# Kernel tuning notes

Hardware: AMD Instinct MI355X
Metric: run time of the kernel (lower is better)

The kernel has to match this reference:

```python
import jax, jax.numpy as jnp
import numpy as np
import math

D_MODEL = 512
NHEAD = 8
D_K = D_MODEL // NHEAD
FACTOR = 5


def setup_inputs() -> dict:
    key = jax.random.key(0)
    ks = jax.random.split(key, 9)
    B, L = 2, 2048
    s = 1.0 / math.sqrt(D_MODEL)
    inp = {
        "x": jax.random.normal(ks[0], (B, L, D_MODEL), dtype=jnp.float32),
        "Wq": jax.random.normal(ks[1], (D_MODEL, D_MODEL), dtype=jnp.float32) * s,
        "bq": jnp.zeros((D_MODEL,), dtype=jnp.float32),
        "Wk": jax.random.normal(ks[2], (D_MODEL, D_MODEL), dtype=jnp.float32) * s,
        "bk": jnp.zeros((D_MODEL,), dtype=jnp.float32),
        "Wv": jax.random.normal(ks[3], (D_MODEL, D_MODEL), dtype=jnp.float32) * s,
        "bv": jnp.zeros((D_MODEL,), dtype=jnp.float32),
        "Wo": jax.random.normal(ks[4], (D_MODEL, D_MODEL), dtype=jnp.float32) * s,
        "bo": jnp.zeros((D_MODEL,), dtype=jnp.float32),
    }
    return inp


def reference(x, Wq, bq, Wk, bk, Wv, bv, Wo, bo):
    B, L, _ = x.shape
    # u keys kept per query (static: depends only on static L)
    u = min(L, int(FACTOR * math.log(L)) if L > 1 else L)

    def proj(W, b):
        # [B,L,D] -> [B,H,L,d_k]
        y = x @ W.T + b
        return y.reshape(B, L, NHEAD, D_K).transpose(0, 2, 1, 3)

    Q = proj(Wq, bq)
    K = proj(Wk, bk)
    V = proj(Wv, bv)

    scores = jnp.einsum("bhqd,bhkd->bhqk", Q, K) / math.sqrt(D_K)  # [B,H,L,L]
    # topk thresholding: keep only scores >= u-th largest per query row
    topk_vals, _ = jax.lax.top_k(scores, u)
    thresh = topk_vals[..., -1:]
    scores = jnp.where(scores < thresh, -10000.0, scores)
    attn = jax.nn.softmax(scores, axis=-1)  # dropout disabled (p=0 / eval)
    out = jnp.einsum("bhqk,bhkd->bhqd", attn, V)  # [B,H,L,d_k]
    out = out.transpose(0, 2, 1, 3).reshape(B, L, D_MODEL)
    return out @ Wo.T + bo
```

## Files before the change

### kernel.cpp

```cpp
#include <hip/hip_runtime.h>
#include <hip/hip_fp16.h>
#include <math.h>

#define LSEQ   2048
#define DMODEL 512
#define NHEAD  8
#define DK     64
#define UK     38

typedef __attribute__((ext_vector_type(8))) _Float16 v8h;
typedef __attribute__((ext_vector_type(4))) _Float16 v4h;
typedef __attribute__((ext_vector_type(4))) float    v4f;

__device__ __forceinline__ unsigned long long mapu64(double x){
    unsigned long long s = (unsigned long long)__double_as_longlong(x);
    return (s & 0x8000000000000000ull) ? ~s : (s | 0x8000000000000000ull);
}
__device__ __forceinline__ unsigned map32(float x){
    unsigned s = __float_as_uint(x);
    return (s & 0x80000000u) ? ~s : (s | 0x80000000u);
}
__device__ __forceinline__ float unmap32(unsigned u){
    unsigned s = (u & 0x80000000u) ? (u & 0x7fffffffu) : ~u;
    return __uint_as_float(s);
}
__device__ __forceinline__ unsigned map16(unsigned h){
    return (h & 0x8000u) ? ((~h) & 0xFFFFu) : (h | 0x8000u);
}

__global__ __launch_bounds__(256) void split_hl(
    const float* __restrict__ X,  const float* __restrict__ Wq,
    const float* __restrict__ Wk, const float* __restrict__ Wv,
    _Float16* __restrict__ Xh, _Float16* __restrict__ Xl,
    _Float16* __restrict__ Whl)
{
    const int idx = blockIdx.x * 256 + threadIdx.x;
    const int NXQ = (4096 * 512) / 4;
    const float* __restrict__ src;
    _Float16* __restrict__ dh;
    _Float16* __restrict__ dl;
    size_t off;
    if (idx < NXQ){
        src = X; dh = Xh; dl = Xl; off = (size_t)idx * 4;
    } else {
        int wi = idx - NXQ;
        int m  = wi >> 16;
        src = (m == 0) ? Wq : (m == 1 ? Wk : Wv);
        dh  = Whl + (size_t)m * 524288;
        dl  = dh + 262144;
        off = (size_t)(wi & 65535) * 4;
    }
    float4 v = *(const float4*)&src[off];
    v4h h, l;
    h[0] = (_Float16)v.x; l[0] = (_Float16)(v.x - (float)h[0]);
    h[1] = (_Float16)v.y; l[1] = (_Float16)(v.y - (float)h[1]);
    h[2] = (_Float16)v.z; l[2] = (_Float16)(v.z - (float)h[2]);
    h[3] = (_Float16)v.w; l[3] = (_Float16)(v.w - (float)h[3]);
    *(v4h*)&dh[off] = h;
    *(v4h*)&dl[off] = l;
}

__global__ __launch_bounds__(256) void qkv_f16(
    const _Float16* __restrict__ Xh, const _Float16* __restrict__ Xl,
    const _Float16* __restrict__ Whl,
    const float* __restrict__ bq, const float* __restrict__ bk,
    const float* __restrict__ bv,
    double* __restrict__ qD, double* __restrict__ kRow,
    __half* __restrict__ qH, __half* __restrict__ kH, float* __restrict__ vB)
{
    const int mode = blockIdx.z;
    const _Float16* __restrict__ Wh = Whl + (size_t)mode * 524288;
    const _Float16* __restrict__ Wl = Wh + 262144;
    const float* __restrict__ bias = (mode == 0) ? bq : (mode == 1 ? bk : bv);
    const int r0 = blockIdx.x * 64, c0 = blockIdx.y * 64;
    __shared__ _Float16 Ah[64][72], Al[64][72];
    __shared__ _Float16 Bh[64][72], Bl[64][72];
    const int tid  = threadIdx.x;
    const int lane = tid & 63, wv = tid >> 6;
    const int m0   = wv << 4;
    const int row  = lane & 15, kq = lane >> 4;

    v4f acc[4] = {};

    for (int kb = 0; kb < DMODEL; kb += 64){
        __syncthreads();
        #pragma unroll
        for (int it = 0; it < 2; ++it){
            int slot = it * 256 + tid;
            int m = slot >> 3, o8 = (slot & 7) << 3;
            size_t ga = (size_t)(r0 + m) * DMODEL + kb + o8;
            size_t gb = (size_t)(c0 + m) * DMODEL + kb + o8;
            *(v8h*)&Ah[m][o8] = *(const v8h*)&Xh[ga];
            *(v8h*)&Al[m][o8] = *(const v8h*)&Xl[ga];
            *(v8h*)&Bh[m][o8] = *(const v8h*)&Wh[gb];
            *(v8h*)&Bl[m][o8] = *(const v8h*)&Wl[gb];
        }
        __syncthreads();
        v8h ah0 = *(const v8h*)&Ah[m0 + row][kq * 8];
        v8h ah1 = *(const v8h*)&Ah[m0 + row][kq * 8 + 32];
        v8h al0 = *(const v8h*)&Al[m0 + row][kq * 8];
        v8h al1 = *(const v8h*)&Al[m0 + row][kq * 8 + 32];
        #pragma unroll
        for (int j = 0; j < 4; ++j){
            const int j0 = j << 4;
            v8h bh0 = *(const v8h*)&Bh[j0 + row][kq * 8];
            v8h bh1 = *(const v8h*)&Bh[j0 + row][kq * 8 + 32];
            v8h bl0 = *(const v8h*)&Bl[j0 + row][kq * 8];
            v8h bl1 = *(const v8h*)&Bl[j0 + row][kq * 8 + 32];
            acc[j] = __builtin_amdgcn_mfma_f32_16x16x32_f16(ah0, bh0, acc[j], 0, 0, 0);
            acc[j] = __builtin_amdgcn_mfma_f32_16x16x32_f16(ah0, bl0, acc[j], 0, 0, 0);
            acc[j] = __builtin_amdgcn_mfma_f32_16x16x32_f16(al0, bh0, acc[j], 0, 0, 0);
            acc[j] = __builtin_amdgcn_mfma_f32_16x16x32_f16(ah1, bh1, acc[j], 0, 0, 0);
            acc[j] = __builtin_amdgcn_mfma_f32_16x16x32_f16(ah1, bl1, acc[j], 0, 0, 0);
            acc[j] = __builtin_amdgcn_mfma_f32_16x16x32_f16(al1, bh1, acc[j], 0, 0, 0);
        }
    }

    const int h = c0 >> 6;
    #pragma unroll
    for (int j = 0; j < 4; ++j){
        const int dk = (j << 4) + row;
        const float bi = bias[c0 + dk];
        #pragma unroll
        for (int rr = 0; rr < 4; ++rr){
            const int r = r0 + m0 + (kq << 2) + rr;
            const int bidx = r >> 11, l = r & 2047;
            const size_t rowb = (size_t)(bidx * NHEAD + h) * LSEQ + l;
            float v = acc[j][rr] + bi;
            if (mode == 0){
                double vd = (double)v * 0.125;
                qD[rowb * DK + dk] = vd;
                ((_Float16*)qH)[rowb * DK + dk] = (_Float16)vd;
            } else if (mode == 1){
                kRow[rowb * DK + dk] = (double)v;
                ((_Float16*)kH)[rowb * DK + dk] = (_Float16)v;
            } else {
                vB[rowb * DK + dk] = v;
            }
        }
    }
}

__global__ __launch_bounds__(256) void gemm_f32(
    const float* __restrict__ X, const float* __restrict__ W,
    const float* __restrict__ bias, float* __restrict__ out)
{
    const int r0 = blockIdx.x * 64, c0 = blockIdx.y * 64;
    __shared__ float Xs[32][68];
    __shared__ float Ws[32][68];
    const int tid = threadIdx.x;
    const int tx = tid & 15, ty = tid >> 4;
    float acc[4][4] = {};
    for (int kb = 0; kb < DMODEL; kb += 32){
        __syncthreads();
        #pragma unroll
        for (int i = 0; i < 2; ++i){
            int f4 = i * 256 + tid;
            int m = f4 >> 3, kg = (f4 & 7) << 2;
            float4 xv = *(const float4*)&X[(r0 + m) * DMODEL + kb + kg];
            Xs[kg+0][m] = xv.x; Xs[kg+1][m] = xv.y; Xs[kg+2][m] = xv.z; Xs[kg+3][m] = xv.w;
            float4 wv = *(const float4*)&W[(c0 + m) * DMODEL + kb + kg];
            Ws[kg+0][m] = wv.x; Ws[kg+1][m] = wv.y; Ws[kg+2][m] = wv.z; Ws[kg+3][m] = wv.w;
        }
        __syncthreads();
        #pragma unroll
        for (int kk = 0; kk < 32; ++kk){
            float4 av = *(const float4*)&Xs[kk][ty << 2];
            float4 bv = *(const float4*)&Ws[kk][tx << 2];
            float a[4] = {av.x, av.y, av.z, av.w};
            float b[4] = {bv.x, bv.y, bv.z, bv.w};
            #pragma unroll
            for (int ii = 0; ii < 4; ++ii)
                #pragma unroll
                for (int jj = 0; jj < 4; ++jj)
                    acc[ii][jj] = fmaf(a[ii], b[jj], acc[ii][jj]);
        }
    }
    #pragma unroll
    for (int ii = 0; ii < 4; ++ii){
        int r = r0 + (ty << 2) + ii;
        float4 o;
        o.x = acc[ii][0] + bias[c0 + (tx << 2) + 0];
        o.y = acc[ii][1] + bias[c0 + (tx << 2) + 1];
        o.z = acc[ii][2] + bias[c0 + (tx << 2) + 2];
        o.w = acc[ii][3] + bias[c0 + (tx << 2) + 3];
        *(float4*)&out[(size_t)r * DMODEL + c0 + (tx << 2)] = o;
    }
}

__global__ __launch_bounds__(256) void score_gemm(
    const __half* __restrict__ qH, const __half* __restrict__ kH,
    __half* __restrict__ Sh, const int bh0)
{
    const int bh = bh0 + blockIdx.z;
    const int r0 = blockIdx.x * 64, c0 = blockIdx.y * 64;
    __shared__ _Float16 Qs[64][72];
    __shared__ _Float16 Ks[64][72];
    const int tid = threadIdx.x;
    const int lane = tid & 63, wv = tid >> 6;
    const size_t qb = ((size_t)bh * LSEQ + r0) * DK;
    const size_t kb = ((size_t)bh * LSEQ + c0) * DK;
    #pragma unroll
    for (int i = 0; i < 2; ++i){
        int c = i * 256 + tid;
        int m = c >> 3, off8 = (c & 7) << 3;
        *(v8h*)&Qs[m][off8] = *(const v8h*)&qH[qb + (size_t)m * DK + off8];
        *(v8h*)&Ks[m][off8] = *(const v8h*)&kH[kb + (size_t)m * DK + off8];
    }
    __syncthreads();
    const int m0 = wv << 4;
    const int row = lane & 15, kq = lane >> 4;
    v8h a0 = *(const v8h*)&Qs[m0 + row][kq * 8];
    v8h a1 = *(const v8h*)&Qs[m0 + row][kq * 8 + 32];
    #pragma unroll
    for (int j0 = 0; j0 < 64; j0 += 16){
        v8h b0 = *(const v8h*)&Ks[j0 + row][kq * 8];
        v8h b1 = *(const v8h*)&Ks[j0 + row][kq * 8 + 32];
        v4f acc = {0.f, 0.f, 0.f, 0.f};
        acc = __builtin_amdgcn_mfma_f32_16x16x32_f16(a0, b0, acc, 0, 0, 0);
        acc = __builtin_amdgcn_mfma_f32_16x16x32_f16(a1, b1, acc, 0, 0, 0);
        #pragma unroll
        for (int r = 0; r < 4; ++r){
            int gr = r0 + m0 + kq * 4 + r;
            int gc = c0 + j0 + row;
            unsigned hbits = (unsigned)__half_as_ushort((__half)acc[r]);
            unsigned short key = (unsigned short)map16(hbits);
            ((unsigned short*)Sh)[((size_t)blockIdx.z * LSEQ + gr) * LSEQ + gc] = key;
        }
    }
}

__device__ __forceinline__ void finish_common(
    const int ncand, const int gl, const int bh, const int lane,
    const double qd, const double* __restrict__ kRow, const float* __restrict__ vB,
    float* __restrict__ ctx, int* __restrict__ jlsR, float* __restrict__ wlsR,
    double* __restrict__ sLds)
{
    const unsigned long long mlt = (1ull << lane) - 1ull;
    if (lane >= ncand) jlsR[lane] = 0;
    if (lane < 4) jlsR[64 + lane] = 0;
    int myJ = jlsR[lane];

    double q8[8];
    #pragma unroll
    for (int k = 0; k < 8; ++k) q8[k] = __shfl(qd, (lane & 7) + (k << 3));
    const int grp = lane >> 3, dl = lane & 7;
    const size_t kb = (size_t)bh * LSEQ;

    double kbf[8];
    {
        int j0 = __shfl(myJ, grp);
        const double* __restrict__ kr = &kRow[(kb + j0) * DK + dl];
        #pragma unroll
        for (int k = 0; k < 8; ++k) kbf[k] = kr[k << 3];
    }
    #pragma unroll
    for (int p = 0; p < 8; ++p){
        double nbf[8];
        if (p < 7){
            int jn = __shfl(myJ, ((p + 1) << 3) + grp);
            const double* __restrict__ krn = &kRow[(kb + jn) * DK + dl];
            #pragma unroll
            for (int k = 0; k < 8; ++k) nbf[k] = krn[k << 3];
        }
        double s = 0.0;
        #pragma unroll
        for (int k = 0; k < 8; ++k) s = fma(q8[k], kbf[k], s);
        s += __shfl_xor(s, 1); s += __shfl_xor(s, 2); s += __shfl_xor(s, 4);
        if (dl == 0) sLds[(p << 3) + grp] = s;
        #pragma unroll
        for (int k = 0; k < 8; ++k) kbf[k] = nbf[k];
    }
    double myS = (lane < ncand) ? sLds[lane] : -1.0e308;

    unsigned long long cu = (lane < ncand) ? mapu64(myS) : 0ull;
    unsigned long long T64 = 0ull;
    for (int bit = 63; bit >= 0; --bit){
        unsigned long long Tp = T64 | (1ull << bit);
        int c = __popcll(__ballot(cu >= Tp));
        if (c >= UK){ T64 = Tp; if (c == UK) break; }
    }
    const bool sel = (cu >= T64);

    double xm = sel ? myS : -1.0e308;
    #pragma unroll
    for (int off = 32; off; off >>= 1) xm = fmax(xm, __shfl_xor(xm, off));
    float w = sel ? expf((float)(myS - xm)) : 0.0f;
    float z = w;
    #pragma unroll
    for (int off = 32; off; off >>= 1) z += __shfl_xor(z, off);
    unsigned long long bm = __ballot(sel);
    int p = __popcll(bm & mlt);
    if (sel){ wlsR[p] = w; jlsR[p] = myJ; }
    const int cnt = __popcll(bm);
    const float invZ = 1.0f / z;

    if (lane >= cnt) wlsR[lane] = 0.0f;
    if (lane < 4){ wlsR[64 + lane] = 0.0f; jlsR[64 + lane] = 0; }

    const float* __restrict__ vsl = vB + (size_t)bh * (LSEQ * DK);
    float o = 0.0f;
    for (int e0 = 0; e0 < cnt; e0 += 16){
        float w16[16]; int j16[16];
        #pragma unroll
        for (int t = 0; t < 16; ++t){ w16[t] = wlsR[e0 + t]; j16[t] = jlsR[e0 + t]; }
        float v16[16];
        #pragma unroll
        for (int t = 0; t < 16; ++t) v16[t] = vsl[(size_t)j16[t] * DK + lane];
        #pragma unroll
        for (int t = 0; t < 16; ++t) o = fmaf(w16[t], v16[t], o);
    }
    ctx[((size_t)(bh >> 3) * LSEQ + gl) * DMODEL + (bh & 7) * DK + lane] = o * invZ;
}

__device__ __forceinline__ void finish_row_f32(
    float (&acc)[32], const int gl, const int bh, const int lane, const float margin,
    const double qd, const double* __restrict__ kRow, const float* __restrict__ vB,
    float* __restrict__ ctx, int* __restrict__ jlsR, float* __restrict__ wlsR,
    double* __restrict__ sLds)
{
    unsigned u[32];
    #pragma unroll
    for (int ch = 0; ch < 32; ++ch) u[ch] = map32(acc[ch]);
    unsigned T = 0u; int curc = 2048;
    for (int bit = 31; bit >= 0; --bit){
        unsigned Tp = T | (1u << bit);
        int c = 0;
        #pragma unroll
        for (int ch = 0; ch < 32; ++ch) c += __popcll(__ballot(u[ch] >= Tp));
        if (c >= UK){ T = Tp; curc = c; }
        if (curc <= 48) break;
    }
    const unsigned Tlo = map32(unmap32(T) - margin);
    const unsigned long long mlt = (1ull << lane) - 1ull;
    int base = 0;
    #pragma unroll
    for (int ch = 0; ch < 32; ++ch){
        bool sel = (u[ch] >= Tlo);
        unsigned long long bm = __ballot(sel);
        int p = base + __popcll(bm & mlt);
        if (sel && p < 64) jlsR[p] = (ch << 6) + lane;
        base += __popcll(bm);
    }
    const int ncand = base > 64 ? 64 : base;
    finish_common(ncand, gl, bh, lane, qd, kRow, vB, ctx, jlsR, wlsR, sLds);
}

__global__ __launch_bounds__(256) void select_kernel(
    const __half* __restrict__ Sh, const double* __restrict__ qD,
    const double* __restrict__ kRow, const float* __restrict__ vB,
    float* __restrict__ ctx, const int bh0)
{
    __shared__ int    jls[4][68];
    __shared__ float  wls[4][68];
    __shared__ double sds[4][64];
    const int tid = threadIdx.x, lane = tid & 63, wv = tid >> 6;
    const int rgS = blockIdx.x * 4 + wv;
    const int bh = bh0 + (rgS >> 11), l = rgS & 2047;
    const double qd = qD[((size_t)bh * LSEQ + l) * DK + lane];
    unsigned u[32];
    const unsigned short* __restrict__ Srow =
        (const unsigned short*)Sh + (size_t)rgS * LSEQ;
    #pragma unroll
    for (int it = 0; it < 4; ++it){
        uint4 v = *(const uint4*)&Srow[it * 512 + (lane << 3)];
        unsigned ws[4] = {v.x, v.y, v.z, v.w};
        #pragma unroll
        for (int q = 0; q < 4; ++q){
            u[it*8 + 2*q]     = ws[q] & 0xFFFFu;
            u[it*8 + 2*q + 1] = ws[q] >> 16;
        }
    }
    unsigned T = 0u; int curc = 2048;
    for (int bit = 15; bit >= 0; --bit){
        unsigned Tp = T | (1u << bit);
        int c = 0;
        #pragma unroll
        for (int ch = 0; ch < 32; ++ch) c += __popcll(__ballot(u[ch] >= Tp));
        if (c >= UK){ T = Tp; curc = c; }
        if (curc <= 48) break;
    }
    unsigned hb = (T & 0x8000u) ? (T & 0x7FFFu) : ((~T) & 0xFFFFu);
    float tf = __half2float(__ushort_as_half((unsigned short)hb)) - 2.2e-2f;
    unsigned short tlb = __half_as_ushort(__float2half_rd(tf));
    const unsigned Tlo = map16(tlb);

    const unsigned long long mlt = (1ull << lane) - 1ull;
    int base = 0;
    #pragma unroll
    for (int ch = 0; ch < 32; ++ch){
        bool sel = (u[ch] >= Tlo);
        unsigned long long bm = __ballot(sel);
        int p = base + __popcll(bm & mlt);
        int j = ((ch >> 3) << 9) + (lane << 3) + (ch & 7);
        if (sel && p < 64) jls[wv][p] = j;
        base += __popcll(bm);
    }
    const int ncand = base > 64 ? 64 : base;
    finish_common(ncand, l, bh, lane, qd, kRow, vB, ctx,
                  &jls[wv][0], &wls[wv][0], &sds[wv][0]);
}

__global__ __launch_bounds__(256) void attn_kernel(
    const double* __restrict__ qD, const double* __restrict__ kRow,
    const float* __restrict__ vB, float* __restrict__ ctx)
{
    __shared__ float2 Kld2[16 * 66];
    __shared__ float  qsf[8][64];
    __shared__ int    jls[8][68];
    __shared__ float  wlsf[8][68];
    __shared__ double sds[8][64];

    const int tid = threadIdx.x, lane = tid & 63, wv = tid >> 6;
    const int bh = blockIdx.x >> 8;
    const int l0 = (blockIdx.x & 255) << 3;
    const int rA = l0 + (wv << 1), rB = rA + 1;

    for (int e = tid; e < 512; e += 256){
        int r = e >> 6, d = e & 63;
        qsf[r][d] = (float)qD[((size_t)bh * LSEQ + l0 + r) * DK + d];
    }
    const double qdA = qD[((size_t)bh * LSEQ + rA) * DK + lane];
    const double qdB = qD[((size_t)bh * LSEQ + rB) * DK + lane];

    float accA[32] = {}, accB[32] = {};
    const size_t kBase = (size_t)bh * (LSEQ * DK);

    for (int dh = 0; dh < 2; ++dh){
        __syncthreads();
        float qa[32], qb[32];
        #pragma unroll
        for (int i = 0; i < 8; ++i){
            float4 va = *(const float4*)&qsf[wv << 1][dh * 32 + i * 4];
            qa[i*4+0]=va.x; qa[i*4+1]=va.y; qa[i*4+2]=va.z; qa[i*4+3]=va.w;
            float4 vb4 = *(const float4*)&qsf[(wv << 1) + 1][dh * 32 + i * 4];
            qb[i*4+0]=vb4.x; qb[i*4+1]=vb4.y; qb[i*4+2]=vb4.z; qb[i*4+3]=vb4.w;
        }
        #pragma unroll
        for (int ch = 0; ch < 32; ++ch){
            const int cb = ch << 6;
            __syncthreads();
            #pragma unroll
            for (int i = 0; i < 4; ++i){
                int j   = i * 16 + (wv << 2) + (lane >> 4);
                int dpl = lane & 15;
                double2 kd = *(const double2*)&kRow[kBase + (size_t)(cb + j) * DK + dh * 32 + dpl * 2];
                Kld2[dpl * 66 + j] = make_float2((float)kd.x, (float)kd.y);
            }
            __syncthreads();
            float a0 = accA[ch], b0 = accB[ch];
            #pragma unroll
            for (int dpl = 0; dpl < 16; ++dpl){
                float2 k = Kld2[dpl * 66 + lane];
                a0 = fmaf(qa[2*dpl],   k.x, a0);
                a0 = fmaf(qa[2*dpl+1], k.y, a0);
                b0 = fmaf(qb[2*dpl],   k.x, b0);
                b0 = fmaf(qb[2*dpl+1], k.y, b0);
            }
            accA[ch] = a0; accB[ch] = b0;
        }
    }

    finish_row_f32(accA, rA, bh, lane, 1e-3f, qdA, kRow, vB, ctx,
                   &jls[wv<<1][0], &wlsf[wv<<1][0], &sds[wv<<1][0]);
    finish_row_f32(accB, rB, bh, lane, 1e-3f, qdB, kRow, vB, ctx,
                   &jls[(wv<<1)+1][0], &wlsf[(wv<<1)+1][0], &sds[(wv<<1)+1][0]);
}

extern "C" void kernel_launch(void* const* d_in, const int* in_sizes, int n_in,
                              void* d_out, int out_size, void* d_ws, size_t ws_size,
                              hipStream_t stream)
{
    const float* x  = (const float*)d_in[0];
    const float* Wq = (const float*)d_in[1];
    const float* bq = (const float*)d_in[2];
    const float* Wk = (const float*)d_in[3];
    const float* bk = (const float*)d_in[4];
    const float* Wv = (const float*)d_in[5];
    const float* bv = (const float*)d_in[6];
    const float* Wo = (const float*)d_in[7];
    const float* bo = (const float*)d_in[8];
    float* out = (float*)d_out;
    char* ws = (char*)d_ws;
    const size_t MiB = 1024 * 1024;
    double* qD   = (double*)(ws);
    double* kRow = (double*)(ws + 16 * MiB);
    float*  vB   = (float*) (ws + 32 * MiB);
    float*  ctx  = (float*) (ws + 40 * MiB);
    __half* qH   = (__half*)(ws + 48 * MiB);
    __half* kH   = (__half*)(ws + 52 * MiB);
    __half* Sh   = (__half*)(ws + 56 * MiB);
    _Float16* Xh  = (_Float16*)(ws + 40 * MiB);
    _Float16* Xl  = (_Float16*)(ws + 44 * MiB);
    _Float16* Whl = (_Float16*)(ws + 56 * MiB);
    size_t avail = (ws_size > 56 * MiB) ? (ws_size - 56 * MiB) : 0;
    int slab = (int)(avail / (8 * MiB)); if (slab > 16) slab = 16;

    dim3 blk(256);
    split_hl<<<dim3(2816), blk, 0, stream>>>(x, Wq, Wk, Wv, Xh, Xl, Whl);
    qkv_f16 <<<dim3(64, 8, 3), blk, 0, stream>>>(Xh, Xl, Whl, bq, bk, bv,
                                                 qD, kRow, qH, kH, vB);
    if (slab >= 1){
        for (int s0 = 0; s0 < NHEAD * 2; s0 += slab){
            int nb = NHEAD * 2 - s0; if (nb > slab) nb = slab;
            score_gemm   <<<dim3(32, 32, nb), blk, 0, stream>>>(qH, kH, Sh, s0);
            select_kernel<<<dim3(nb * 512),   blk, 0, stream>>>(Sh, qD, kRow, vB, ctx, s0);
        }
    } else {
        attn_kernel<<<dim3(4096), blk, 0, stream>>>(qD, kRow, vB, ctx);
    }
    gemm_f32<<<dim3(64, 8), blk, 0, stream>>>(ctx, Wo, bo, out);
}
```

Baseline: 279.1 us.

## Replace bitwise radix threshold search with LDS histogram select in select_kernel

The per-row top-k threshold search used a 16-step bitwise loop, where each step ran 32 ballots over the row's fp16 keys. It is replaced with a 256-bin LDS histogram on the high byte, a wave prefix scan to find the bin holding the k-th largest key, and a bitwise search over only the keys in that bin. The old loop is kept as a fallback when that bin holds more than 64 keys. Separately, finish_common's software-pipelined K gather over a fixed 8 chunks becomes a simple loop over only ncand candidates, giving up prefetch overlap in exchange for skipping unused chunks. The histogram adds LDS atomics whose contention depends on how the keys are distributed, and the finished threshold can differ slightly from the old search's early-exit threshold.

```diff
diff --git a/kernel.cpp b/kernel.cpp
--- a/kernel.cpp
+++ b/kernel.cpp
@@ -246,30 +246,14 @@
     for (int k = 0; k < 8; ++k) q8[k] = __shfl(qd, (lane & 7) + (k << 3));
     const int grp = lane >> 3, dl = lane & 7;
     const size_t kb = (size_t)bh * LSEQ;
-
-    double kbf[8];
-    {
-        int j0 = __shfl(myJ, grp);
-        const double* __restrict__ kr = &kRow[(kb + j0) * DK + dl];
-        #pragma unroll
-        for (int k = 0; k < 8; ++k) kbf[k] = kr[k << 3];
-    }
-    #pragma unroll
-    for (int p = 0; p < 8; ++p){
-        double nbf[8];
-        if (p < 7){
-            int jn = __shfl(myJ, ((p + 1) << 3) + grp);
-            const double* __restrict__ krn = &kRow[(kb + jn) * DK + dl];
-            #pragma unroll
-            for (int k = 0; k < 8; ++k) nbf[k] = krn[k << 3];
-        }
+    for (int e0 = 0; e0 < ncand; e0 += 8){
+        int j = jlsR[e0 + grp];
+        const double* __restrict__ kr = &kRow[(kb + j) * DK + dl];
         double s = 0.0;
         #pragma unroll
-        for (int k = 0; k < 8; ++k) s = fma(q8[k], kbf[k], s);
+        for (int k = 0; k < 8; ++k) s = fma(q8[k], kr[k << 3], s);
         s += __shfl_xor(s, 1); s += __shfl_xor(s, 2); s += __shfl_xor(s, 4);
-        if (dl == 0) sLds[(p << 3) + grp] = s;
-        #pragma unroll
-        for (int k = 0; k < 8; ++k) kbf[k] = nbf[k];
+        if (dl == 0) sLds[e0 + grp] = s;
     }
     double myS = (lane < ncand) ? sLds[lane] : -1.0e308;
 
@@ -351,13 +335,21 @@
     const double* __restrict__ kRow, const float* __restrict__ vB,
     float* __restrict__ ctx, const int bh0)
 {
-    __shared__ int    jls[4][68];
-    __shared__ float  wls[4][68];
-    __shared__ double sds[4][64];
+    __shared__ int      jls[4][68];
+    __shared__ float    wls[4][68];
+    __shared__ double   sds[4][64];
+    __shared__ unsigned hist[4][256];
+    __shared__ unsigned cbuf[4][64];
+    __shared__ unsigned ccnt[4];
     const int tid = threadIdx.x, lane = tid & 63, wv = tid >> 6;
     const int rgS = blockIdx.x * 4 + wv;
     const int bh = bh0 + (rgS >> 11), l = rgS & 2047;
     const double qd = qD[((size_t)bh * LSEQ + l) * DK + lane];
+
+    #pragma unroll
+    for (int k = 0; k < 4; ++k) hist[wv][(lane << 2) + k] = 0u;
+    if (lane == 0) ccnt[wv] = 0u;
+
     unsigned u[32];
     const unsigned short* __restrict__ Srow =
         (const unsigned short*)Sh + (size_t)rgS * LSEQ;
@@ -371,15 +363,66 @@
             u[it*8 + 2*q + 1] = ws[q] >> 16;
         }
     }
-    unsigned T = 0u; int curc = 2048;
-    for (int bit = 15; bit >= 0; --bit){
-        unsigned Tp = T | (1u << bit);
-        int c = 0;
-        #pragma unroll
-        for (int ch = 0; ch < 32; ++ch) c += __popcll(__ballot(u[ch] >= Tp));
-        if (c >= UK){ T = Tp; curc = c; }
-        if (curc <= 48) break;
-    }
+
+    #pragma unroll
+    for (int ch = 0; ch < 32; ++ch) atomicAdd(&hist[wv][u[ch] >> 8], 1u);
+
+    int c4[4];
+    #pragma unroll
+    for (int k = 0; k < 4; ++k) c4[k] = (int)hist[wv][(lane << 2) + k];
+    int sl = c4[0] + c4[1] + c4[2] + c4[3];
+    int t = sl;
+    #pragma unroll
+    for (int off = 1; off < 64; off <<= 1){
+        int v = __shfl_down(t, off);
+        if (lane + off < 64) t += v;
+    }
+    const int aboveGroup = t - sl;
+    int ab[4];
+    ab[3] = aboveGroup;
+    ab[2] = ab[3] + c4[3];
+    ab[1] = ab[2] + c4[2];
+    ab[0] = ab[1] + c4[1];
+    int foundk = -1;
+    #pragma unroll
+    for (int k = 0; k < 4; ++k)
+        if (ab[k] < UK && UK <= ab[k] + c4[k]) foundk = k;
+    unsigned long long fb = __ballot(foundk >= 0);
+    const int srcLane = __ffsll((long long)fb) - 1;
+    const int bstar  = __shfl((lane << 2) + (foundk >= 0 ? foundk : 0), srcLane);
+    const int nAbove = __shfl(foundk >= 0 ? ab[foundk] : 0, srcLane);
+    const int bcnt   = (int)hist[wv][bstar];
+    const int kth    = UK - nAbove;
+
+    unsigned T;
+    if (bcnt <= 64){
+        #pragma unroll
+        for (int ch = 0; ch < 32; ++ch){
+            if ((int)(u[ch] >> 8) == bstar){
+                unsigned p = atomicAdd(&ccnt[wv], 1u);
+                if (p < 64u) cbuf[wv][p] = u[ch];
+            }
+        }
+        const int nb = (int)ccnt[wv];
+        unsigned key = (lane < nb) ? cbuf[wv][lane] : 0u;
+        T = 0u;
+        for (int bit = 15; bit >= 0; --bit){
+            unsigned Tp = T | (1u << bit);
+            int c = __popcll(__ballot(lane < nb && key >= Tp));
+            if (c >= kth) T = Tp;
+        }
+    } else {
+        T = 0u; int curc = 2048;
+        for (int bit = 15; bit >= 0; --bit){
+            unsigned Tp = T | (1u << bit);
+            int c = 0;
+            #pragma unroll
+            for (int ch = 0; ch < 32; ++ch) c += __popcll(__ballot(u[ch] >= Tp));
+            if (c >= UK){ T = Tp; curc = c; }
+            if (curc <= 48) break;
+        }
+    }
+
     unsigned hb = (T & 0x8000u) ? (T & 0x7FFFu) : ((~T) & 0xFFFFu);
     float tf = __half2float(__ushort_as_half((unsigned short)hb)) - 2.2e-2f;
     unsigned short tlb = __half_as_ushort(__float2half_rd(tf));
```

Measured after the change: 278.3 us. No clear change (-0.3%).
